# Kernel optimization log

Measured on AMD Instinct MI355X. Metric: run time of the kernel, lower is better.

The kernel has to match this reference:

```python
import jax, jax.numpy as jnp
import numpy as np

N_HEAD = 16
D_K = 64
D_MODEL = N_HEAD * D_K
LN_EPS = 1e-5


def setup_inputs() -> dict:
    key = jax.random.key(0)
    ks = jax.random.split(key, 11)
    B, Tq, Tk = 4, 2048, 2048
    s = 1.0 / np.sqrt(D_MODEL)
    return {
        "q": jax.random.normal(ks[0], (B, Tq, D_MODEL), jnp.float32),
        "k": jax.random.normal(ks[1], (B, Tk, D_MODEL), jnp.float32),
        "v": jax.random.normal(ks[2], (B, Tk, D_MODEL), jnp.float32),
        "Wq": jax.random.normal(ks[3], (D_MODEL, D_MODEL), jnp.float32) * s,
        "bq": jnp.zeros((D_MODEL,), jnp.float32),
        "Wk": jax.random.normal(ks[4], (D_MODEL, D_MODEL), jnp.float32) * s,
        "bk": jnp.zeros((D_MODEL,), jnp.float32),
        "Wv": jax.random.normal(ks[5], (D_MODEL, D_MODEL), jnp.float32) * s,
        "bv": jnp.zeros((D_MODEL,), jnp.float32),
        "Wo": jax.random.normal(ks[6], (D_MODEL, D_MODEL), jnp.float32) * s,
        "bo": jnp.zeros((D_MODEL,), jnp.float32),
        "gamma": jnp.ones((D_MODEL,), jnp.float32),
        "beta": jnp.zeros((D_MODEL,), jnp.float32),
    }


def reference(q, k, v, Wq, bq, Wk, bk, Wv, bv, Wo, bo, gamma, beta):
    B, Tq, _ = q.shape
    Tk = k.shape[1]
    temperature = jnp.asarray(D_K ** 0.5, q.dtype)

    # projections (torch Linear: x @ W.T + b), reshape to heads: [B, T, H, DK]
    qh = (q @ Wq.T + bq).reshape(B, Tq, N_HEAD, D_K)
    kh = (k @ Wk.T + bk).reshape(B, Tk, N_HEAD, D_K)
    vh = (v @ Wv.T + bv).reshape(B, Tk, N_HEAD, D_K)

    # scores [B, H, Tq, Tk]; softmax over Tk (dropout is identity in eval)
    scores = jnp.einsum('bqhd,bkhd->bhqk', qh, kh) / temperature
    attn = jax.nn.softmax(scores, axis=-1)

    # attention output -> concat heads [B, Tq, D_MODEL]
    out = jnp.einsum('bhqk,bkhd->bqhd', attn, vh).reshape(B, Tq, D_MODEL)

    out = out @ Wo.T + bo
    x = out + q  # residual
    mu = jnp.mean(x, axis=-1, keepdims=True)
    var = jnp.var(x, axis=-1, keepdims=True)
    out_norm = (x - mu) * jax.lax.rsqrt(var + LN_EPS) * gamma + beta

    # attn returned in torch layout [NHead*B, Tq, Tk]
    attn_flat = attn.transpose(1, 0, 2, 3).reshape(N_HEAD * B, Tq, Tk)
    return (out_norm, attn_flat)
```

## Files before the change

### kernel.cpp

```cpp
#include <hip/hip_runtime.h>
#include <cstdint>
#include <cstddef>

typedef __attribute__((ext_vector_type(4))) float f32x4;
typedef __attribute__((ext_vector_type(8))) short s16x8;
typedef __attribute__((ext_vector_type(4))) unsigned short u16x4;
typedef __attribute__((ext_vector_type(8))) unsigned short u16x8;

#define MFMA16(a, b, c) __builtin_amdgcn_mfma_f32_16x16x32_bf16((a), (b), (c), 0, 0, 0)
#define GLOAD_LDS16(src, dst)                                             \
  __builtin_amdgcn_global_load_lds(                                       \
      (const __attribute__((address_space(1))) void*)(src),               \
      (__attribute__((address_space(3))) void*)(dst), 16, 0, 0)

static constexpr int kD = 1024;
static constexpr int kT = 2048;

__device__ __forceinline__ unsigned short f2bf(float f) {
  union { float f; uint32_t u; } v; v.f = f;
  uint32_t r = v.u + 0x7fffu + ((v.u >> 16) & 1u);
  return (unsigned short)(r >> 16);
}
__device__ __forceinline__ float bf2f(unsigned short h) {
  union { float f; uint32_t u; } v; v.u = ((uint32_t)h) << 16;
  return v.f;
}

__global__ __launch_bounds__(256) void convert_split_k(
    const float* __restrict__ src, unsigned short* __restrict__ hi,
    unsigned short* __restrict__ lo, int n4) {
  for (int i = blockIdx.x * 256 + threadIdx.x; i < n4; i += gridDim.x * 256) {
    f32x4 v = ((const f32x4*)src)[i];
    u16x4 h4, l4;
#pragma unroll
    for (int j = 0; j < 4; j++) {
      h4[j] = f2bf(v[j]);
      l4[j] = f2bf(v[j] - bf2f(h4[j]));
    }
    ((u16x4*)hi)[i] = h4;
    ((u16x4*)lo)[i] = l4;
  }
}

__global__ __launch_bounds__(256) void convert_plain_k(
    const float* __restrict__ src, unsigned short* __restrict__ dst, int n4) {
  for (int i = blockIdx.x * 256 + threadIdx.x; i < n4; i += gridDim.x * 256) {
    f32x4 v = ((const f32x4*)src)[i];
    u16x4 h4;
#pragma unroll
    for (int j = 0; j < 4; j++) h4[j] = f2bf(v[j]);
    ((u16x4*)dst)[i] = h4;
  }
}

template <int MODE, int MINW>
__global__ __launch_bounds__(256, MINW) void gemm_bf16(
    const unsigned short* __restrict__ Xhi, const unsigned short* __restrict__ Xlo,
    const unsigned short* __restrict__ Whi, const unsigned short* __restrict__ Wlo,
    const float* __restrict__ bias, const float* __restrict__ resid,
    unsigned short* __restrict__ outHi, unsigned short* __restrict__ outLo,
    float* __restrict__ outF, float oscale) {
  constexpr bool SPLIT = (MODE == 0);
  __shared__ unsigned short smem[(SPLIT ? 4 : 2) * 128 * 64];
  unsigned short* Ah = smem;
  unsigned short* Bh = smem + 8192;
  unsigned short* Al = SPLIT ? smem + 16384 : smem;
  unsigned short* Bl = SPLIT ? smem + 24576 : smem;

  const int tid = threadIdx.x, lane = tid & 63, w = tid >> 6;
  const int wg = (blockIdx.x & 7) * 64 + (blockIdx.x >> 3);
  const int m0 = (wg >> 3) * 128, n0 = (wg & 7) * 128;
  const int wm0 = (w >> 1) * 64, wn0 = (w & 1) * 64;
  const int lr = lane & 15, lk = lane >> 4;
  const int srow = lane >> 3, sslot = (lane & 7) ^ srow;

  const size_t xoff = (size_t)(m0 + w * 32 + srow) * kD + sslot * 8;
  const size_t woff = (size_t)(n0 + w * 32 + srow) * kD + sslot * 8;

  f32x4 acc[4][4];
#pragma unroll
  for (int i = 0; i < 4; i++)
#pragma unroll
    for (int j = 0; j < 4; j++) acc[i][j] = (f32x4){0.f, 0.f, 0.f, 0.f};

  for (int kt = 0; kt < kD / 64; ++kt) {
    __syncthreads();
    const int kof = kt * 64;
#pragma unroll
    for (int i = 0; i < 4; i++) {
      const int ldst = (w * 32 + i * 8) * 64;
      GLOAD_LDS16(Xhi + xoff + (size_t)i * 8 * kD + kof, &Ah[ldst]);
      GLOAD_LDS16(Whi + woff + (size_t)i * 8 * kD + kof, &Bh[ldst]);
      if constexpr (SPLIT) {
        GLOAD_LDS16(Xlo + xoff + (size_t)i * 8 * kD + kof, &Al[ldst]);
        GLOAD_LDS16(Wlo + woff + (size_t)i * 8 * kD + kof, &Bl[ldst]);
      }
    }
    __syncthreads();
#pragma unroll
    for (int ks = 0; ks < 2; ks++) {
      s16x8 af[4], bf[4], al[4], bl[4];
#pragma unroll
      for (int i = 0; i < 4; i++) {
        const int ra = wm0 + i * 16 + lr;
        const int oa = ra * 128 + ((((ks * 4) + lk) ^ (ra & 7)) << 4);
        const int rb = wn0 + i * 16 + lr;
        const int ob = rb * 128 + ((((ks * 4) + lk) ^ (rb & 7)) << 4);
        af[i] = *(const s16x8*)((const char*)Ah + oa);
        bf[i] = *(const s16x8*)((const char*)Bh + ob);
        if constexpr (SPLIT) {
          al[i] = *(const s16x8*)((const char*)Al + oa);
          bl[i] = *(const s16x8*)((const char*)Bl + ob);
        }
      }
#pragma unroll
      for (int i = 0; i < 4; i++)
#pragma unroll
        for (int j = 0; j < 4; j++) {
          if constexpr (SPLIT) {
            acc[i][j] = MFMA16(al[i], bf[j], acc[i][j]);
            acc[i][j] = MFMA16(af[i], bl[j], acc[i][j]);
          }
          acc[i][j] = MFMA16(af[i], bf[j], acc[i][j]);
        }
    }
  }

#pragma unroll
  for (int j = 0; j < 4; j++) {
    const int col = n0 + wn0 + j * 16 + lr;
    const float bv = bias[col];
#pragma unroll
    for (int i = 0; i < 4; i++)
#pragma unroll
      for (int r = 0; r < 4; r++) {
        const int row = m0 + wm0 + i * 16 + lk * 4 + r;
        const size_t idx = (size_t)row * kD + col;
        float vv = acc[i][j][r] + bv;
        if constexpr (MODE == 0) {
          vv *= oscale;
          unsigned short h = f2bf(vv);
          outHi[idx] = h;
          outLo[idx] = f2bf(vv - bf2f(h));
        } else if constexpr (MODE == 1) {
          outHi[idx] = f2bf(vv);
        } else {
          outF[idx] = vv + resid[idx];
        }
      }
  }
}

__global__ __launch_bounds__(256) void transpose_v(
    const unsigned short* __restrict__ vh, unsigned short* __restrict__ vhT) {
  __shared__ unsigned short lds[64 * 72];
  const int bx = blockIdx.x;
  const int tt = bx & 31, bhp = bx >> 5;
  const int b = bhp >> 4, h = bhp & 15;
  const int t0 = tt * 64, tid = threadIdx.x;
  {
    const int t = tid >> 2, c0 = (tid & 3) * 16;
    const unsigned short* src = &vh[(size_t)(b * kT + t0 + t) * kD + h * 64 + c0];
    u16x8 v0 = *(const u16x8*)src;
    u16x8 v1 = *(const u16x8*)(src + 8);
    *(u16x8*)&lds[t * 72 + c0] = v0;
    *(u16x8*)&lds[t * 72 + c0 + 8] = v1;
  }
  __syncthreads();
  {
    const int d = tid >> 2, tc0 = (tid & 3) * 16;
    u16x8 o0, o1;
#pragma unroll
    for (int i = 0; i < 8; i++) o0[i] = lds[(tc0 + i) * 72 + d];
#pragma unroll
    for (int i = 0; i < 8; i++) o1[i] = lds[(tc0 + 8 + i) * 72 + d];
    size_t base = ((size_t)((b * 16 + h) * 64 + d)) * kT + t0 + tc0;
    *(u16x8*)&vhT[base] = o0;
    *(u16x8*)&vhT[base + 8] = o1;
  }
}

__global__ __launch_bounds__(256, 2) void attn_fused(
    const unsigned short* __restrict__ qhi, const unsigned short* __restrict__ qlo,
    const unsigned short* __restrict__ khi, const unsigned short* __restrict__ klo,
    const unsigned short* __restrict__ vhT, unsigned short* __restrict__ attn_out,
    float* __restrict__ attn_p) {
  __shared__ unsigned short q_hi[128 * 64], q_lo[128 * 64];
  __shared__ unsigned short k_hi[64 * 64], k_lo[64 * 64];
  __shared__ unsigned short vt[64 * 64];
  __shared__ unsigned short p_lds[4][32 * 72];

  const int tid = threadIdx.x, lane = tid & 63, w = tid >> 6;
  const int lr = lane & 15, lk = lane >> 4;
  const int srow = lane >> 3, sslot = (lane & 7) ^ srow;
  const int wg = (blockIdx.x & 7) * 128 + (blockIdx.x >> 3);
  const int bh = wg >> 4, qt = wg & 15;
  const int h = bh >> 2, b = bh & 3;
  const int q0 = qt * 128;
  const int qm0 = w * 32;

  const size_t qsrc = (size_t)(b * kT + q0 + w * 32 + srow) * kD + h * 64 + sslot * 8;
#pragma unroll
  for (int i = 0; i < 4; i++) {
    const int ldst = (w * 32 + i * 8) * 64;
    GLOAD_LDS16(qhi + qsrc + (size_t)i * 8 * kD, &q_hi[ldst]);
    GLOAD_LDS16(qlo + qsrc + (size_t)i * 8 * kD, &q_lo[ldst]);
  }

  const size_t kbase = (size_t)(b * kT + w * 16 + srow) * kD + h * 64 + sslot * 8;
  const size_t vbase = ((size_t)((b * 16 + h) * 64) + w * 16 + srow) * kT + sslot * 8;

  s16x8 qfh[2][2];
  float l_s[2][4];
#pragma unroll
  for (int mi = 0; mi < 2; mi++)
#pragma unroll
    for (int r = 0; r < 4; r++) l_s[mi][r] = 0.f;

  for (int kt = 0; kt < kT / 64; ++kt) {
    __syncthreads();
#pragma unroll
    for (int i = 0; i < 2; i++) {
      const int ldst = (w * 16 + i * 8) * 64;
      GLOAD_LDS16(khi + kbase + (size_t)(kt * 64 + i * 8) * kD, &k_hi[ldst]);
    }
    __syncthreads();
    if (kt == 0) {
#pragma unroll
      for (int mi = 0; mi < 2; mi++)
#pragma unroll
        for (int ks = 0; ks < 2; ks++) {
          const int rq = qm0 + mi * 16 + lr;
          const int oq = rq * 128 + ((((ks * 4) + lk) ^ (rq & 7)) << 4);
          qfh[mi][ks] = *(const s16x8*)((const char*)q_hi + oq);
        }
    }
    f32x4 sc[2][4];
#pragma unroll
    for (int mi = 0; mi < 2; mi++)
#pragma unroll
      for (int ni = 0; ni < 4; ni++) sc[mi][ni] = (f32x4){0.f, 0.f, 0.f, 0.f};
#pragma unroll
    for (int ks = 0; ks < 2; ks++) {
      s16x8 kfh[4];
#pragma unroll
      for (int ni = 0; ni < 4; ni++) {
        const int rk = ni * 16 + lr;
        const int ok = rk * 128 + ((((ks * 4) + lk) ^ (rk & 7)) << 4);
        kfh[ni] = *(const s16x8*)((const char*)k_hi + ok);
      }
#pragma unroll
      for (int mi = 0; mi < 2; mi++)
#pragma unroll
        for (int ni = 0; ni < 4; ni++)
          sc[mi][ni] = MFMA16(qfh[mi][ks], kfh[ni], sc[mi][ni]);
    }
#pragma unroll
    for (int mi = 0; mi < 2; mi++)
#pragma unroll
      for (int r = 0; r < 4; r++) {
        float s = __expf(sc[mi][0][r]) + __expf(sc[mi][1][r]) +
                  __expf(sc[mi][2][r]) + __expf(sc[mi][3][r]);
#pragma unroll
        for (int d = 1; d < 16; d <<= 1) s += __shfl_xor(s, d, 64);
        l_s[mi][r] += s;
      }
  }

  float rl[2][4];
#pragma unroll
  for (int mi = 0; mi < 2; mi++)
#pragma unroll
    for (int r = 0; r < 4; r++) rl[mi][r] = 1.0f / l_s[mi][r];

  s16x8 qfl[2][2];
#pragma unroll
  for (int mi = 0; mi < 2; mi++)
#pragma unroll
    for (int ks = 0; ks < 2; ks++) {
      const int rq = qm0 + mi * 16 + lr;
      const int oq = rq * 128 + ((((ks * 4) + lk) ^ (rq & 7)) << 4);
      qfl[mi][ks] = *(const s16x8*)((const char*)q_lo + oq);
    }

  f32x4 pv[2][4];
#pragma unroll
  for (int mi = 0; mi < 2; mi++)
#pragma unroll
    for (int ni = 0; ni < 4; ni++) pv[mi][ni] = (f32x4){0.f, 0.f, 0.f, 0.f};

  for (int kt = 0; kt < kT / 64; ++kt) {
    __syncthreads();
#pragma unroll
    for (int i = 0; i < 2; i++) {
      const int ldst = (w * 16 + i * 8) * 64;
      const size_t so = kbase + (size_t)(kt * 64 + i * 8) * kD;
      GLOAD_LDS16(khi + so, &k_hi[ldst]);
      GLOAD_LDS16(klo + so, &k_lo[ldst]);
      GLOAD_LDS16(vhT + vbase + (size_t)i * 8 * kT + kt * 64, &vt[ldst]);
    }
    __syncthreads();
    f32x4 sc[2][4];
#pragma unroll
    for (int mi = 0; mi < 2; mi++)
#pragma unroll
      for (int ni = 0; ni < 4; ni++) sc[mi][ni] = (f32x4){0.f, 0.f, 0.f, 0.f};
#pragma unroll
    for (int ks = 0; ks < 2; ks++) {
      s16x8 kfh[4], kfl[4];
#pragma unroll
      for (int ni = 0; ni < 4; ni++) {
        const int rk = ni * 16 + lr;
        const int ok = rk * 128 + ((((ks * 4) + lk) ^ (rk & 7)) << 4);
        kfh[ni] = *(const s16x8*)((const char*)k_hi + ok);
        kfl[ni] = *(const s16x8*)((const char*)k_lo + ok);
      }
#pragma unroll
      for (int mi = 0; mi < 2; mi++)
#pragma unroll
        for (int ni = 0; ni < 4; ni++) {
          sc[mi][ni] = MFMA16(qfl[mi][ks], kfh[ni], sc[mi][ni]);
          sc[mi][ni] = MFMA16(qfh[mi][ks], kfl[ni], sc[mi][ni]);
          sc[mi][ni] = MFMA16(qfh[mi][ks], kfh[ni], sc[mi][ni]);
        }
    }
#pragma unroll
    for (int mi = 0; mi < 2; mi++)
#pragma unroll
      for (int ni = 0; ni < 4; ni++)
#pragma unroll
        for (int r = 0; r < 4; r++) {
          const float p = __expf(sc[mi][ni][r]) * rl[mi][r];
          const int qrow = q0 + qm0 + mi * 16 + lk * 4 + r;
          __builtin_nontemporal_store(
              p, &attn_p[((size_t)(bh * kT + qrow)) * kT + kt * 64 + ni * 16 + lr]);
          p_lds[w][(mi * 16 + lk * 4 + r) * 72 + ni * 16 + lr] = f2bf(p);
        }
    __syncthreads();
#pragma unroll
    for (int ks = 0; ks < 2; ks++) {
      s16x8 pf[2], vf[4];
#pragma unroll
      for (int mi = 0; mi < 2; mi++)
        pf[mi] = *(const s16x8*)&p_lds[w][(mi * 16 + lr) * 72 + ks * 32 + lk * 8];
#pragma unroll
      for (int ni = 0; ni < 4; ni++) {
        const int row = ni * 16 + lr;
        const int sw2 = ((ks * 4) + lk) ^ (row & 7);
        vf[ni] = *(const s16x8*)((const char*)vt + row * 128 + (sw2 << 4));
      }
#pragma unroll
      for (int mi = 0; mi < 2; mi++)
#pragma unroll
        for (int ni = 0; ni < 4; ni++)
          pv[mi][ni] = MFMA16(pf[mi], vf[ni], pv[mi][ni]);
    }
  }

#pragma unroll
  for (int mi = 0; mi < 2; mi++)
#pragma unroll
    for (int ni = 0; ni < 4; ni++)
#pragma unroll
      for (int r = 0; r < 4; r++) {
        const int qrow = q0 + qm0 + mi * 16 + lk * 4 + r;
        attn_out[((size_t)(b * kT + qrow)) * kD + h * 64 + ni * 16 + lr] =
            f2bf(pv[mi][ni][r]);
      }
}

__global__ __launch_bounds__(256) void ln_kernel(
    const float* __restrict__ x, const float* __restrict__ gamma,
    const float* __restrict__ beta, float* __restrict__ out) {
  __shared__ float ssum[4], ssq[4];
  const int row = blockIdx.x, tid = threadIdx.x;
  f32x4 v = *(const f32x4*)&x[(size_t)row * kD + tid * 4];
  float s = v[0] + v[1] + v[2] + v[3];
  float q2 = v[0] * v[0] + v[1] * v[1] + v[2] * v[2] + v[3] * v[3];
#pragma unroll
  for (int d = 1; d < 64; d <<= 1) {
    s += __shfl_xor(s, d, 64);
    q2 += __shfl_xor(q2, d, 64);
  }
  const int w = tid >> 6, lane = tid & 63;
  if (lane == 0) {
    ssum[w] = s;
    ssq[w] = q2;
  }
  __syncthreads();
  s = ssum[0] + ssum[1] + ssum[2] + ssum[3];
  q2 = ssq[0] + ssq[1] + ssq[2] + ssq[3];
  const float mu = s * (1.f / 1024.f);
  const float var = q2 * (1.f / 1024.f) - mu * mu;
  const float rstd = rsqrtf(var + 1e-5f);
  f32x4 g = *(const f32x4*)&gamma[tid * 4];
  f32x4 bb = *(const f32x4*)&beta[tid * 4];
  f32x4 o;
#pragma unroll
  for (int j = 0; j < 4; j++) o[j] = (v[j] - mu) * rstd * g[j] + bb[j];
  *(f32x4*)&out[(size_t)row * kD + tid * 4] = o;
}

extern "C" void kernel_launch(void* const* d_in, const int* in_sizes, int n_in,
                              void* d_out, int out_size, void* d_ws,
                              size_t ws_size, hipStream_t stream) {
  const float* q = (const float*)d_in[0];
  const float* k = (const float*)d_in[1];
  const float* v = (const float*)d_in[2];
  const float* Wq = (const float*)d_in[3];
  const float* bq = (const float*)d_in[4];
  const float* Wk = (const float*)d_in[5];
  const float* bk = (const float*)d_in[6];
  const float* Wv = (const float*)d_in[7];
  const float* bv = (const float*)d_in[8];
  const float* Wo = (const float*)d_in[9];
  const float* bo = (const float*)d_in[10];
  const float* gamma = (const float*)d_in[11];
  const float* beta = (const float*)d_in[12];

  float* out = (float*)d_out;
  float* attn_p = out + (size_t)8192 * 1024;

  constexpr size_t NQ = (size_t)4 * 2048 * 1024;
  constexpr size_t NW = (size_t)1024 * 1024;

  unsigned short* w16 = (unsigned short*)d_ws;
  unsigned short* q_hi = w16 + 0 * NQ;
  unsigned short* q_lo = w16 + 1 * NQ;
  unsigned short* k_hi = w16 + 2 * NQ;
  unsigned short* k_lo = w16 + 3 * NQ;
  unsigned short* v_b  = w16 + 4 * NQ;
  unsigned short* qh_hi = w16 + 5 * NQ;
  unsigned short* qh_lo = w16 + 6 * NQ;
  unsigned short* kh_hi = w16 + 7 * NQ;
  unsigned short* kh_lo = w16 + 8 * NQ;
  unsigned short* vh_b  = w16 + 9 * NQ;
  unsigned short* vhT   = w16 + 10 * NQ;
  unsigned short* ao_b  = w16 + 11 * NQ;
  unsigned short* Wq_hi = w16 + 12 * NQ;
  unsigned short* Wq_lo = Wq_hi + NW;
  unsigned short* Wk_hi = Wq_hi + 2 * NW;
  unsigned short* Wk_lo = Wq_hi + 3 * NW;
  unsigned short* Wv_b  = Wq_hi + 4 * NW;
  unsigned short* Wo_b  = Wq_hi + 5 * NW;
  float* xbuf = (float*)(Wq_hi + 6 * NW);

  dim3 blk(256);
  convert_split_k<<<4096, blk, 0, stream>>>(q, q_hi, q_lo, (int)(NQ / 4));
  convert_split_k<<<4096, blk, 0, stream>>>(k, k_hi, k_lo, (int)(NQ / 4));
  convert_plain_k<<<4096, blk, 0, stream>>>(v, v_b, (int)(NQ / 4));
  convert_split_k<<<1024, blk, 0, stream>>>(Wq, Wq_hi, Wq_lo, (int)(NW / 4));
  convert_split_k<<<1024, blk, 0, stream>>>(Wk, Wk_hi, Wk_lo, (int)(NW / 4));
  convert_plain_k<<<1024, blk, 0, stream>>>(Wv, Wv_b, (int)(NW / 4));
  convert_plain_k<<<1024, blk, 0, stream>>>(Wo, Wo_b, (int)(NW / 4));

  gemm_bf16<0, 2><<<512, blk, 0, stream>>>(q_hi, q_lo, Wq_hi, Wq_lo, bq, nullptr,
                                           qh_hi, qh_lo, nullptr, 0.125f);
  gemm_bf16<0, 2><<<512, blk, 0, stream>>>(k_hi, k_lo, Wk_hi, Wk_lo, bk, nullptr,
                                           kh_hi, kh_lo, nullptr, 1.0f);
  gemm_bf16<1, 3><<<512, blk, 0, stream>>>(v_b, nullptr, Wv_b, nullptr, bv, nullptr,
                                           vh_b, nullptr, nullptr, 1.0f);
  transpose_v<<<2048, blk, 0, stream>>>(vh_b, vhT);
  attn_fused<<<1024, blk, 0, stream>>>(qh_hi, qh_lo, kh_hi, kh_lo, vhT, ao_b,
                                       attn_p);
  gemm_bf16<2, 3><<<512, blk, 0, stream>>>(ao_b, nullptr, Wo_b, nullptr, bo, q,
                                           nullptr, nullptr, xbuf, 1.0f);
  ln_kernel<<<8192, blk, 0, stream>>>(xbuf, gamma, beta, out);
}
```

Before: 607.4 us.

## Drop hi/lo split for projected Q/K and double-buffer K/V in attention

The Q and K projection GEMMs now write a single bf16 output instead of hi/lo pairs. The attention kernel computes scores with one MFMA per tile instead of three in the second pass. K and V tiles are double-buffered in LDS so the next tile's global loads overlap compute, and the per-row sum shuffle-reduction is moved out of the loop. This cuts MFMA work, memory traffic and barriers, but score accuracy falls to plain bf16, which could exceed the tolerance on the attention probabilities.

```diff
diff --git a/kernel.cpp b/kernel.cpp
--- a/kernel.cpp
+++ b/kernel.cpp
@@ -58,8 +58,7 @@
     const unsigned short* __restrict__ Xhi, const unsigned short* __restrict__ Xlo,
     const unsigned short* __restrict__ Whi, const unsigned short* __restrict__ Wlo,
     const float* __restrict__ bias, const float* __restrict__ resid,
-    unsigned short* __restrict__ outHi, unsigned short* __restrict__ outLo,
-    float* __restrict__ outF, float oscale) {
+    unsigned short* __restrict__ outB, float* __restrict__ outF, float oscale) {
   constexpr bool SPLIT = (MODE == 0);
   __shared__ unsigned short smem[(SPLIT ? 4 : 2) * 128 * 64];
   unsigned short* Ah = smem;
@@ -138,12 +137,9 @@
         const size_t idx = (size_t)row * kD + col;
         float vv = acc[i][j][r] + bv;
         if constexpr (MODE == 0) {
-          vv *= oscale;
-          unsigned short h = f2bf(vv);
-          outHi[idx] = h;
-          outLo[idx] = f2bf(vv - bf2f(h));
+          outB[idx] = f2bf(vv * oscale);
         } else if constexpr (MODE == 1) {
-          outHi[idx] = f2bf(vv);
+          outB[idx] = f2bf(vv);
         } else {
           outF[idx] = vv + resid[idx];
         }
@@ -181,14 +177,12 @@
 }
 
 __global__ __launch_bounds__(256, 2) void attn_fused(
-    const unsigned short* __restrict__ qhi, const unsigned short* __restrict__ qlo,
-    const unsigned short* __restrict__ khi, const unsigned short* __restrict__ klo,
+    const unsigned short* __restrict__ qh, const unsigned short* __restrict__ kh,
     const unsigned short* __restrict__ vhT, unsigned short* __restrict__ attn_out,
     float* __restrict__ attn_p) {
-  __shared__ unsigned short q_hi[128 * 64], q_lo[128 * 64];
-  __shared__ unsigned short k_hi[64 * 64], k_lo[64 * 64];
-  __shared__ unsigned short vt[64 * 64];
-  __shared__ unsigned short p_lds[4][32 * 72];
+  __shared__ unsigned short kbuf[2][64 * 64];
+  __shared__ unsigned short vbuf[2][64 * 64];
+  __shared__ unsigned short qp[9216];
 
   const int tid = threadIdx.x, lane = tid & 63, w = tid >> 6;
   const int lr = lane & 15, lk = lane >> 4;
@@ -196,45 +190,45 @@
   const int wg = (blockIdx.x & 7) * 128 + (blockIdx.x >> 3);
   const int bh = wg >> 4, qt = wg & 15;
   const int h = bh >> 2, b = bh & 3;
-  const int q0 = qt * 128;
-  const int qm0 = w * 32;
+  const int q0 = qt * 128, qm0 = w * 32;
 
   const size_t qsrc = (size_t)(b * kT + q0 + w * 32 + srow) * kD + h * 64 + sslot * 8;
 #pragma unroll
-  for (int i = 0; i < 4; i++) {
-    const int ldst = (w * 32 + i * 8) * 64;
-    GLOAD_LDS16(qhi + qsrc + (size_t)i * 8 * kD, &q_hi[ldst]);
-    GLOAD_LDS16(qlo + qsrc + (size_t)i * 8 * kD, &q_lo[ldst]);
-  }
+  for (int i = 0; i < 4; i++)
+    GLOAD_LDS16(qh + qsrc + (size_t)i * 8 * kD, &qp[(w * 32 + i * 8) * 64]);
 
   const size_t kbase = (size_t)(b * kT + w * 16 + srow) * kD + h * 64 + sslot * 8;
   const size_t vbase = ((size_t)((b * 16 + h) * 64) + w * 16 + srow) * kT + sslot * 8;
 
-  s16x8 qfh[2][2];
-  float l_s[2][4];
+#pragma unroll
+  for (int i = 0; i < 2; i++)
+    GLOAD_LDS16(kh + kbase + (size_t)(i * 8) * kD, &kbuf[0][(w * 16 + i * 8) * 64]);
+  __syncthreads();
+
+  s16x8 qf[2][2];
 #pragma unroll
   for (int mi = 0; mi < 2; mi++)
 #pragma unroll
-    for (int r = 0; r < 4; r++) l_s[mi][r] = 0.f;
+    for (int ks = 0; ks < 2; ks++) {
+      const int rq = qm0 + mi * 16 + lr;
+      qf[mi][ks] = *(const s16x8*)((const char*)qp + rq * 128 +
+                                   ((((ks * 4) + lk) ^ (rq & 7)) << 4));
+    }
+
+  float l_part[2][4];
+#pragma unroll
+  for (int mi = 0; mi < 2; mi++)
+#pragma unroll
+    for (int r = 0; r < 4; r++) l_part[mi][r] = 0.f;
 
   for (int kt = 0; kt < kT / 64; ++kt) {
-    __syncthreads();
-#pragma unroll
-    for (int i = 0; i < 2; i++) {
-      const int ldst = (w * 16 + i * 8) * 64;
-      GLOAD_LDS16(khi + kbase + (size_t)(kt * 64 + i * 8) * kD, &k_hi[ldst]);
-    }
-    __syncthreads();
-    if (kt == 0) {
-#pragma unroll
-      for (int mi = 0; mi < 2; mi++)
-#pragma unroll
-        for (int ks = 0; ks < 2; ks++) {
-          const int rq = qm0 + mi * 16 + lr;
-          const int oq = rq * 128 + ((((ks * 4) + lk) ^ (rq & 7)) << 4);
-          qfh[mi][ks] = *(const s16x8*)((const char*)q_hi + oq);
-        }
-    }
+    if (kt + 1 < kT / 64) {
+#pragma unroll
+      for (int i = 0; i < 2; i++)
+        GLOAD_LDS16(kh + kbase + (size_t)((kt + 1) * 64 + i * 8) * kD,
+                    &kbuf[(kt + 1) & 1][(w * 16 + i * 8) * 64]);
+    }
+    const unsigned short* kb = kbuf[kt & 1];
     f32x4 sc[2][4];
 #pragma unroll
     for (int mi = 0; mi < 2; mi++)
@@ -242,87 +236,86 @@
       for (int ni = 0; ni < 4; ni++) sc[mi][ni] = (f32x4){0.f, 0.f, 0.f, 0.f};
 #pragma unroll
     for (int ks = 0; ks < 2; ks++) {
-      s16x8 kfh[4];
+      s16x8 kf[4];
 #pragma unroll
       for (int ni = 0; ni < 4; ni++) {
         const int rk = ni * 16 + lr;
-        const int ok = rk * 128 + ((((ks * 4) + lk) ^ (rk & 7)) << 4);
-        kfh[ni] = *(const s16x8*)((const char*)k_hi + ok);
+        kf[ni] = *(const s16x8*)((const char*)kb + rk * 128 +
+                                 ((((ks * 4) + lk) ^ (rk & 7)) << 4));
       }
 #pragma unroll
       for (int mi = 0; mi < 2; mi++)
 #pragma unroll
         for (int ni = 0; ni < 4; ni++)
-          sc[mi][ni] = MFMA16(qfh[mi][ks], kfh[ni], sc[mi][ni]);
+          sc[mi][ni] = MFMA16(qf[mi][ks], kf[ni], sc[mi][ni]);
     }
 #pragma unroll
     for (int mi = 0; mi < 2; mi++)
 #pragma unroll
-      for (int r = 0; r < 4; r++) {
-        float s = __expf(sc[mi][0][r]) + __expf(sc[mi][1][r]) +
-                  __expf(sc[mi][2][r]) + __expf(sc[mi][3][r]);
-#pragma unroll
-        for (int d = 1; d < 16; d <<= 1) s += __shfl_xor(s, d, 64);
-        l_s[mi][r] += s;
-      }
+      for (int r = 0; r < 4; r++)
+        l_part[mi][r] += __expf(sc[mi][0][r]) + __expf(sc[mi][1][r]) +
+                         __expf(sc[mi][2][r]) + __expf(sc[mi][3][r]);
+    __syncthreads();
   }
 
   float rl[2][4];
 #pragma unroll
   for (int mi = 0; mi < 2; mi++)
 #pragma unroll
-    for (int r = 0; r < 4; r++) rl[mi][r] = 1.0f / l_s[mi][r];
-
-  s16x8 qfl[2][2];
+    for (int r = 0; r < 4; r++) {
+      float s = l_part[mi][r];
+#pragma unroll
+      for (int d = 1; d < 16; d <<= 1) s += __shfl_xor(s, d, 64);
+      rl[mi][r] = 1.0f / s;
+    }
+
+  f32x4 pv[2][4];
 #pragma unroll
   for (int mi = 0; mi < 2; mi++)
 #pragma unroll
+    for (int ni = 0; ni < 4; ni++) pv[mi][ni] = (f32x4){0.f, 0.f, 0.f, 0.f};
+
+#pragma unroll
+  for (int i = 0; i < 2; i++) {
+    const int ldst = (w * 16 + i * 8) * 64;
+    GLOAD_LDS16(kh + kbase + (size_t)(i * 8) * kD, &kbuf[0][ldst]);
+    GLOAD_LDS16(vhT + vbase + (size_t)i * 8 * kT, &vbuf[0][ldst]);
+  }
+  unsigned short* p_w = &qp[w * 2304];
+  __syncthreads();
+
+  for (int kt = 0; kt < kT / 64; ++kt) {
+    if (kt + 1 < kT / 64) {
+#pragma unroll
+      for (int i = 0; i < 2; i++) {
+        const int ldst = (w * 16 + i * 8) * 64;
+        GLOAD_LDS16(kh + kbase + (size_t)((kt + 1) * 64 + i * 8) * kD,
+                    &kbuf[(kt + 1) & 1][ldst]);
+        GLOAD_LDS16(vhT + vbase + (size_t)i * 8 * kT + (kt + 1) * 64,
+                    &vbuf[(kt + 1) & 1][ldst]);
+      }
+    }
+    const unsigned short* kb = kbuf[kt & 1];
+    const unsigned short* vb = vbuf[kt & 1];
+    f32x4 sc[2][4];
+#pragma unroll
+    for (int mi = 0; mi < 2; mi++)
+#pragma unroll
+      for (int ni = 0; ni < 4; ni++) sc[mi][ni] = (f32x4){0.f, 0.f, 0.f, 0.f};
+#pragma unroll
     for (int ks = 0; ks < 2; ks++) {
-      const int rq = qm0 + mi * 16 + lr;
-      const int oq = rq * 128 + ((((ks * 4) + lk) ^ (rq & 7)) << 4);
-      qfl[mi][ks] = *(const s16x8*)((const char*)q_lo + oq);
-    }
-
-  f32x4 pv[2][4];
-#pragma unroll
-  for (int mi = 0; mi < 2; mi++)
-#pragma unroll
-    for (int ni = 0; ni < 4; ni++) pv[mi][ni] = (f32x4){0.f, 0.f, 0.f, 0.f};
-
-  for (int kt = 0; kt < kT / 64; ++kt) {
-    __syncthreads();
-#pragma unroll
-    for (int i = 0; i < 2; i++) {
-      const int ldst = (w * 16 + i * 8) * 64;
-      const size_t so = kbase + (size_t)(kt * 64 + i * 8) * kD;
-      GLOAD_LDS16(khi + so, &k_hi[ldst]);
-      GLOAD_LDS16(klo + so, &k_lo[ldst]);
-      GLOAD_LDS16(vhT + vbase + (size_t)i * 8 * kT + kt * 64, &vt[ldst]);
-    }
-    __syncthreads();
-    f32x4 sc[2][4];
-#pragma unroll
-    for (int mi = 0; mi < 2; mi++)
-#pragma unroll
-      for (int ni = 0; ni < 4; ni++) sc[mi][ni] = (f32x4){0.f, 0.f, 0.f, 0.f};
-#pragma unroll
-    for (int ks = 0; ks < 2; ks++) {
-      s16x8 kfh[4], kfl[4];
+      s16x8 kf[4];
 #pragma unroll
       for (int ni = 0; ni < 4; ni++) {
         const int rk = ni * 16 + lr;
-        const int ok = rk * 128 + ((((ks * 4) + lk) ^ (rk & 7)) << 4);
-        kfh[ni] = *(const s16x8*)((const char*)k_hi + ok);
-        kfl[ni] = *(const s16x8*)((const char*)k_lo + ok);
+        kf[ni] = *(const s16x8*)((const char*)kb + rk * 128 +
+                                 ((((ks * 4) + lk) ^ (rk & 7)) << 4));
       }
 #pragma unroll
       for (int mi = 0; mi < 2; mi++)
 #pragma unroll
-        for (int ni = 0; ni < 4; ni++) {
-          sc[mi][ni] = MFMA16(qfl[mi][ks], kfh[ni], sc[mi][ni]);
-          sc[mi][ni] = MFMA16(qfh[mi][ks], kfl[ni], sc[mi][ni]);
-          sc[mi][ni] = MFMA16(qfh[mi][ks], kfh[ni], sc[mi][ni]);
-        }
+        for (int ni = 0; ni < 4; ni++)
+          sc[mi][ni] = MFMA16(qf[mi][ks], kf[ni], sc[mi][ni]);
     }
 #pragma unroll
     for (int mi = 0; mi < 2; mi++)
@@ -334,20 +327,19 @@
           const int qrow = q0 + qm0 + mi * 16 + lk * 4 + r;
           __builtin_nontemporal_store(
               p, &attn_p[((size_t)(bh * kT + qrow)) * kT + kt * 64 + ni * 16 + lr]);
-          p_lds[w][(mi * 16 + lk * 4 + r) * 72 + ni * 16 + lr] = f2bf(p);
+          p_w[(mi * 16 + lk * 4 + r) * 72 + ni * 16 + lr] = f2bf(p);
         }
-    __syncthreads();
 #pragma unroll
     for (int ks = 0; ks < 2; ks++) {
       s16x8 pf[2], vf[4];
 #pragma unroll
       for (int mi = 0; mi < 2; mi++)
-        pf[mi] = *(const s16x8*)&p_lds[w][(mi * 16 + lr) * 72 + ks * 32 + lk * 8];
+        pf[mi] = *(const s16x8*)&p_w[(mi * 16 + lr) * 72 + ks * 32 + lk * 8];
 #pragma unroll
       for (int ni = 0; ni < 4; ni++) {
         const int row = ni * 16 + lr;
         const int sw2 = ((ks * 4) + lk) ^ (row & 7);
-        vf[ni] = *(const s16x8*)((const char*)vt + row * 128 + (sw2 << 4));
+        vf[ni] = *(const s16x8*)((const char*)vb + row * 128 + (sw2 << 4));
       }
 #pragma unroll
       for (int mi = 0; mi < 2; mi++)
@@ -355,6 +347,7 @@
         for (int ni = 0; ni < 4; ni++)
           pv[mi][ni] = MFMA16(pf[mi], vf[ni], pv[mi][ni]);
     }
+    __syncthreads();
   }
 
 #pragma unroll
@@ -430,14 +423,12 @@
   unsigned short* k_hi = w16 + 2 * NQ;
   unsigned short* k_lo = w16 + 3 * NQ;
   unsigned short* v_b  = w16 + 4 * NQ;
-  unsigned short* qh_hi = w16 + 5 * NQ;
-  unsigned short* qh_lo = w16 + 6 * NQ;
-  unsigned short* kh_hi = w16 + 7 * NQ;
-  unsigned short* kh_lo = w16 + 8 * NQ;
-  unsigned short* vh_b  = w16 + 9 * NQ;
-  unsigned short* vhT   = w16 + 10 * NQ;
-  unsigned short* ao_b  = w16 + 11 * NQ;
-  unsigned short* Wq_hi = w16 + 12 * NQ;
+  unsigned short* qh_b = w16 + 5 * NQ;
+  unsigned short* kh_b = w16 + 6 * NQ;
+  unsigned short* vh_b = w16 + 7 * NQ;
+  unsigned short* vhT  = w16 + 8 * NQ;
+  unsigned short* ao_b = w16 + 9 * NQ;
+  unsigned short* Wq_hi = w16 + 10 * NQ;
   unsigned short* Wq_lo = Wq_hi + NW;
   unsigned short* Wk_hi = Wq_hi + 2 * NW;
   unsigned short* Wk_lo = Wq_hi + 3 * NW;
@@ -455,15 +446,14 @@
   convert_plain_k<<<1024, blk, 0, stream>>>(Wo, Wo_b, (int)(NW / 4));
 
   gemm_bf16<0, 2><<<512, blk, 0, stream>>>(q_hi, q_lo, Wq_hi, Wq_lo, bq, nullptr,
-                                           qh_hi, qh_lo, nullptr, 0.125f);
+                                           qh_b, nullptr, 0.125f);
   gemm_bf16<0, 2><<<512, blk, 0, stream>>>(k_hi, k_lo, Wk_hi, Wk_lo, bk, nullptr,
-                                           kh_hi, kh_lo, nullptr, 1.0f);
+                                           kh_b, nullptr, 1.0f);
   gemm_bf16<1, 3><<<512, blk, 0, stream>>>(v_b, nullptr, Wv_b, nullptr, bv, nullptr,
-                                           vh_b, nullptr, nullptr, 1.0f);
+                                           vh_b, nullptr, 1.0f);
   transpose_v<<<2048, blk, 0, stream>>>(vh_b, vhT);
-  attn_fused<<<1024, blk, 0, stream>>>(qh_hi, qh_lo, kh_hi, kh_lo, vhT, ao_b,
-                                       attn_p);
+  attn_fused<<<1024, blk, 0, stream>>>(qh_b, kh_b, vhT, ao_b, attn_p);
   gemm_bf16<2, 3><<<512, blk, 0, stream>>>(ao_b, nullptr, Wo_b, nullptr, bo, q,
-                                           nullptr, nullptr, xbuf, 1.0f);
+                                           nullptr, xbuf, 1.0f);
   ln_kernel<<<8192, blk, 0, stream>>>(xbuf, gamma, beta, out);
 }
```

New measurement: 571.5 us. 1.06x faster.
